# Kernel tuning notes

Hardware: AMD Instinct MI355X
Metric: run time of the kernel (lower is better)

## Reference

```python
import jax, jax.numpy as jnp
import numpy as np

B, N, C, CO = 256, 80, 1024, 1024
SLOPE = 0.2
BN_EPS = 1e-5

def leaky(x):
    return jax.nn.leaky_relu(x, SLOPE)

def setup_inputs() -> dict:
    key = jax.random.key(0)
    ks = jax.random.split(key, 8)
    stdv = 1.0 / np.sqrt(C)
    return {
        "x": jax.random.normal(ks[0], (B, N, C), jnp.float32),
        "out1": jax.random.normal(ks[1], (B, N), jnp.float32),
        "A": jax.random.uniform(ks[2], (N, N), jnp.float32, 0.05, 1.0),
        "static_weight": jax.random.uniform(ks[3], (C, C), jnp.float32, -stdv, stdv),
        "conv_g_w": jax.random.normal(ks[4], (C, C), jnp.float32) * 0.02,
        "conv_g_b": jnp.zeros((C,), jnp.float32),
        "bn_gamma": jnp.ones((C,), jnp.float32),
        "bn_beta": jnp.zeros((C,), jnp.float32),
        "conv_co_w": jax.random.normal(ks[5], (N, 2 * C), jnp.float32) * 0.02,
        "conv_co_b": jnp.zeros((N,), jnp.float32),
        "dynamic_weight": jax.random.uniform(ks[6], (C, CO), jnp.float32, -stdv, stdv),
    }

def _gen_adj(A):
    # D = diag(rowsum(A)^-0.5); adj = (A @ D).T @ D = D A^T D
    d = jnp.power(A.sum(1), -0.5)
    return d[:, None] * A.T * d[None, :]

def _gen_adjs(A):
    # batched version of _gen_adj; A: [B,N,N]
    d = jnp.power(A.sum(2), -0.5)  # [B,N]
    return d[:, :, None] * jnp.swapaxes(A, 1, 2) * d[:, None, :]

def reference(x, out1, A, static_weight, conv_g_w, conv_g_b, bn_gamma, bn_beta, conv_co_w, conv_co_b, dynamic_weight):
    n = x.shape[1]
    # static GCN + residual
    adj_s = _gen_adj(A)
    h = leaky(jnp.einsum('ij,bjc->bic', adj_s, x))
    x = x + h @ static_weight
    # construct dynamic graph
    xt = jnp.swapaxes(x, 1, 2)                      # [B,C,N]
    glb = xt.mean(2)                                # adaptive avg pool -> [B,C]
    glb = glb @ conv_g_w.T + conv_g_b               # 1x1 conv
    mu = glb.mean(0)
    var = glb.var(0)                                # biased, training-mode BN
    glb = (glb - mu) * jax.lax.rsqrt(var + BN_EPS) * bn_gamma + bn_beta
    glb = leaky(glb)
    cat = jnp.concatenate([jnp.broadcast_to(glb[:, :, None], xt.shape), xt], axis=1)  # [B,2C,N]
    dyn = jax.nn.sigmoid(jnp.einsum('nk,bkm->bnm', conv_co_w, cat) + conv_co_b[None, :, None])  # [B,N,N]
    # adjacency consistency loss
    out1s = jax.nn.sigmoid(out1)
    t = jnp.einsum('bn,bnm->bm', out1s, dyn) / n
    loss = jnp.sum(jnp.linalg.norm(out1s - t, axis=1))
    # dynamic GCN
    adjs = _gen_adjs(dyn)
    h = leaky(jnp.einsum('bnm,bmc->bnc', adjs, x))
    out = leaky(h @ dynamic_weight)
    return out, loss
```

## Files before the change

kernel.cpp:

```cpp
#include <hip/hip_runtime.h>
#include <hip/hip_bf16.h>
#include <math.h>

#define B_  256
#define N_  80
#define C_  1024
#define CO_ 1024

typedef __hip_bfloat16 bf16;
using bf16x8 = __attribute__((ext_vector_type(8))) short;
using f32x4  = __attribute__((ext_vector_type(4))) float;

__device__ __forceinline__ float leaky(float v){ return v >= 0.f ? v : 0.2f * v; }
__device__ __forceinline__ float sigmoidf_(float v){ return 1.f / (1.f + __expf(-v)); }

__device__ __forceinline__ void gll16(const void* g, void* l){
    __builtin_amdgcn_global_load_lds(
        (const __attribute__((address_space(1))) void*)g,
        (__attribute__((address_space(3))) void*)l, 16, 0, 0);
}

__global__ __launch_bounds__(256) void k_convT2(const float* __restrict__ W0, const float* __restrict__ W1,
                                                bf16* __restrict__ T0, bf16* __restrict__ T1){
    __shared__ float t[32][33];
    const float* W = blockIdx.z ? W1 : W0;
    bf16* WT = blockIdx.z ? T1 : T0;
    int k0 = blockIdx.y * 32, n0 = blockIdx.x * 32;
    int tx = threadIdx.x & 31, ty = threadIdx.x >> 5;
    for (int i = ty; i < 32; i += 8) t[i][tx] = W[(size_t)(k0 + i) * 1024 + n0 + tx];
    __syncthreads();
    for (int i = ty; i < 32; i += 8)
        WT[(size_t)(n0 + i) * 1024 + k0 + tx] = __float2bfloat16(t[tx][i]);
}

__global__ void k_cvt_ccw(const float* __restrict__ ccw, bf16* __restrict__ ccwb){
    int i = blockIdx.x * 256 + threadIdx.x;
    ccwb[i] = __float2bfloat16(ccw[i]);
}
__global__ void k_cvt4(const float* __restrict__ src, bf16* __restrict__ dst){
    int i = (blockIdx.x * 256 + threadIdx.x) * 4;
    float4 v = *(const float4*)(src + i);
    dst[i + 0] = __float2bfloat16(v.x);
    dst[i + 1] = __float2bfloat16(v.y);
    dst[i + 2] = __float2bfloat16(v.z);
    dst[i + 3] = __float2bfloat16(v.w);
}

__global__ void k_adj(const float* __restrict__ A, bf16* __restrict__ adjb){
    __shared__ float d[N_];
    int t = threadIdx.x;
    if (t < N_){
        float s = 0.f;
        for (int j = 0; j < N_; j++) s += A[t * N_ + j];
        d[t] = rsqrtf(s);
    }
    __syncthreads();
    for (int idx = t; idx < N_ * N_; idx += 256){
        int i = idx / N_, j = idx - i * N_;
        adjb[i * 88 + j] = __float2bfloat16(d[i] * A[j * N_ + i] * d[j]);
    }
}

__global__ __launch_bounds__(128) void k_prop_static(const float* __restrict__ xsrc,
                                                     const bf16* __restrict__ Ag,
                                                     bf16* __restrict__ H){
    __shared__ bf16 Btl[128 * 88];
    __shared__ bf16 Al [80 * 88];
    int b = blockIdx.x, c0 = blockIdx.y * 128, tid = threadIdx.x;
    int wave = tid >> 6, lane = tid & 63;
    int l15 = lane & 15, hi = lane >> 4;

    #pragma unroll
    for (int k = 0; k < 7; k++){
        int cb = k * 128 + wave * 64;
        if (cb + lane < 880)
            gll16(Ag + (size_t)(cb + lane) * 8, Al + (size_t)cb * 8);
    }
    {
        size_t rowbase = (size_t)b * 81920 + c0 + tid;
        #pragma unroll 8
        for (int m = 0; m < 80; m++)
            Btl[tid * 88 + m] = __float2bfloat16(xsrc[rowbase + (size_t)m * 1024]);
    }
    __syncthreads();

    f32x4 acc[5][4];
    #pragma unroll
    for (int i = 0; i < 5; i++)
        #pragma unroll
        for (int j = 0; j < 4; j++) acc[i][j] = (f32x4){0.f, 0.f, 0.f, 0.f};

    #pragma unroll
    for (int ks = 0; ks < 3; ks++){
        bf16x8 a[5], bv[4];
        if (ks < 2){
            int k0 = ks * 32;
            #pragma unroll
            for (int i = 0; i < 5; i++)
                a[i] = *(const bf16x8*)(Al + (i * 16 + l15) * 88 + k0 + hi * 8);
            #pragma unroll
            for (int j = 0; j < 4; j++)
                bv[j] = *(const bf16x8*)(Btl + (wave * 64 + j * 16 + l15) * 88 + k0 + hi * 8);
        } else {
            int koff = (hi < 2) ? 64 + hi * 8 : 0;
            #pragma unroll
            for (int i = 0; i < 5; i++){
                bf16x8 v = *(const bf16x8*)(Al + (i * 16 + l15) * 88 + koff);
                if (hi >= 2) v = 0;
                a[i] = v;
            }
            #pragma unroll
            for (int j = 0; j < 4; j++){
                bf16x8 v = *(const bf16x8*)(Btl + (wave * 64 + j * 16 + l15) * 88 + koff);
                if (hi >= 2) v = 0;
                bv[j] = v;
            }
        }
        #pragma unroll
        for (int i = 0; i < 5; i++)
            #pragma unroll
            for (int j = 0; j < 4; j++)
                acc[i][j] = __builtin_amdgcn_mfma_f32_16x16x32_bf16(a[i], bv[j], acc[i][j], 0, 0, 0);
    }

    #pragma unroll
    for (int i = 0; i < 5; i++){
        #pragma unroll
        for (int r = 0; r < 4; r++){
            int orow = i * 16 + hi * 4 + r;
            #pragma unroll
            for (int j = 0; j < 4; j++){
                int ocol = c0 + wave * 64 + j * 16 + l15;
                H[(size_t)b * 81920 + (size_t)orow * 1024 + ocol] =
                    __float2bfloat16(leaky(acc[i][j][r]));
            }
        }
    }
}

template<int EPI>
__global__ __launch_bounds__(256, 4) void k_gemm_mfma(const bf16* __restrict__ Abf,
                                                      const bf16* __restrict__ WT,
                                                      const float* __restrict__ Res,
                                                      void* __restrict__ Outv){
    __shared__ alignas(16) bf16 As[3][128 * 32];
    __shared__ alignas(16) bf16 Bs[2][128 * 32];
    const int K = 1024;
    const int NT = 32;
    int tid = threadIdx.x;
    int wave = tid >> 6, lane = tid & 63;
    int l15 = lane & 15, hi = lane >> 4;

    int bid = blockIdx.x;
    int xcd = bid & 7, idx = bid >> 3;
    int row0 = (xcd * 20 + (idx >> 3)) * 128;
    int col0 = (idx & 7) * 128;

    int sr = tid >> 2;
    int sq = (tid & 3) ^ ((tid >> 3) & 3);
    const bf16* gA = Abf + (size_t)(row0 + sr) * K + sq * 8;
    const bf16* gB = WT  + (size_t)(col0 + sr) * K + sq * 8;

    int wr = (wave >> 1) * 64, wc = (wave & 1) * 64;
    int soff = (hi ^ ((l15 >> 1) & 3)) * 8;

    f32x4 acc[4][4];
    #pragma unroll
    for (int i = 0; i < 4; i++)
        #pragma unroll
        for (int j = 0; j < 4; j++) acc[i][j] = (f32x4){0.f, 0.f, 0.f, 0.f};

    auto STAGE_A = [&](int t){
        bf16* da = &As[t % 3][wave * 512];
        gll16(gA + t * 32, da);
        gll16(gA + (size_t)64 * K + t * 32, da + 2048);
    };
    auto STAGE_B = [&](int t){
        bf16* db = &Bs[t & 1][wave * 512];
        gll16(gB + t * 32, db);
        gll16(gB + (size_t)64 * K + t * 32, db + 2048);
    };

    STAGE_A(0); STAGE_B(0); STAGE_A(1);
    for (int t = 0; t < NT; ++t){
        if (t < NT - 1) asm volatile("s_waitcnt vmcnt(2)" ::: "memory");
        else            asm volatile("s_waitcnt vmcnt(0)" ::: "memory");
        __builtin_amdgcn_s_barrier();
        if (t + 1 < NT) STAGE_B(t + 1);
        if (t + 2 < NT) STAGE_A(t + 2);
        const bf16* pa = &As[t % 3][0] + (wr + l15) * 32 + soff;
        const bf16* pb = &Bs[t & 1][0] + (wc + l15) * 32 + soff;
        bf16x8 a[4], b[4];
        #pragma unroll
        for (int i = 0; i < 4; i++) a[i] = *(const bf16x8*)(pa + i * 512);
        #pragma unroll
        for (int j = 0; j < 4; j++) b[j] = *(const bf16x8*)(pb + j * 512);
        __builtin_amdgcn_s_setprio(1);
        #pragma unroll
        for (int i = 0; i < 4; i++)
            #pragma unroll
            for (int j = 0; j < 4; j++)
                acc[i][j] = __builtin_amdgcn_mfma_f32_16x16x32_bf16(a[i], b[j], acc[i][j], 0, 0, 0);
        __builtin_amdgcn_s_setprio(0);
    }

    int orow = row0 + wr + hi * 4;
    int ocol = col0 + wc + l15;
    #pragma unroll
    for (int i = 0; i < 4; i++){
        #pragma unroll
        for (int r = 0; r < 4; r++){
            int rr = orow + i * 16 + r;
            #pragma unroll
            for (int j = 0; j < 4; j++){
                size_t o = (size_t)rr * 1024 + ocol + j * 16;
                float v = acc[i][j][r];
                if (EPI == 0) ((bf16*)Outv)[o] = __float2bfloat16(v + Res[o]);
                else          ((float*)Outv)[o] = leaky(v);
            }
        }
    }
}

__global__ __launch_bounds__(256) void k_gemm_glb(const bf16* __restrict__ Abf,
                                                  const bf16* __restrict__ Bw,
                                                  const float* __restrict__ bias,
                                                  float* __restrict__ Out){
    __shared__ alignas(16) bf16 As[3][128 * 32];
    __shared__ alignas(16) bf16 Bs[3][128 * 32];
    const int K = 1024;
    const int NT = 32;
    int tid = threadIdx.x;
    int wave = tid >> 6, lane = tid & 63;
    int l15 = lane & 15, hi = lane >> 4;

    int row0 = (blockIdx.x >> 3) * 128;
    int col0 = (blockIdx.x & 7) * 128;

    int sr = tid >> 2;
    int sq = (tid & 3) ^ ((tid >> 3) & 3);
    const bf16* gA = Abf + (size_t)(row0 + sr) * K + sq * 8;
    const bf16* gB = Bw  + (size_t)(col0 + sr) * K + sq * 8;

    int wr = (wave >> 1) * 64, wc = (wave & 1) * 64;
    int soff = (hi ^ ((l15 >> 1) & 3)) * 8;

    f32x4 acc[4][4];
    #pragma unroll
    for (int i = 0; i < 4; i++)
        #pragma unroll
        for (int j = 0; j < 4; j++) acc[i][j] = (f32x4){0.f, 0.f, 0.f, 0.f};

    auto STAGE = [&](int t){
        int buf = t % 3;
        int k0 = t * 32;
        bf16* da = &As[buf][wave * 512];
        bf16* db = &Bs[buf][wave * 512];
        gll16(gA + k0, da);
        gll16(gA + (size_t)64 * K + k0, da + 2048);
        gll16(gB + k0, db);
        gll16(gB + (size_t)64 * K + k0, db + 2048);
    };

    STAGE(0);
    STAGE(1);
    for (int t = 0; t < NT; ++t){
        if (t == NT - 1) asm volatile("s_waitcnt vmcnt(0)" ::: "memory");
        else             asm volatile("s_waitcnt vmcnt(4)" ::: "memory");
        __builtin_amdgcn_s_barrier();
        if (t + 2 < NT) STAGE(t + 2);
        int buf = t % 3;
        const bf16* pa = &As[buf][0] + (wr + l15) * 32 + soff;
        const bf16* pb = &Bs[buf][0] + (wc + l15) * 32 + soff;
        bf16x8 a[4], b[4];
        #pragma unroll
        for (int i = 0; i < 4; i++) a[i] = *(const bf16x8*)(pa + i * 512);
        #pragma unroll
        for (int j = 0; j < 4; j++) b[j] = *(const bf16x8*)(pb + j * 512);
        #pragma unroll
        for (int i = 0; i < 4; i++)
            #pragma unroll
            for (int j = 0; j < 4; j++)
                acc[i][j] = __builtin_amdgcn_mfma_f32_16x16x32_bf16(a[i], b[j], acc[i][j], 0, 0, 0);
    }

    int orow = row0 + wr + hi * 4;
    int ocol = col0 + wc + l15;
    #pragma unroll
    for (int i = 0; i < 4; i++){
        #pragma unroll
        for (int r = 0; r < 4; r++){
            int rr = orow + i * 16 + r;
            #pragma unroll
            for (int j = 0; j < 4; j++){
                int cl = ocol + j * 16;
                Out[(size_t)rr * 1024 + cl] = acc[i][j][r] + bias[cl];
            }
        }
    }
}

__global__ __launch_bounds__(128) void k_pool(const bf16* __restrict__ X2b, bf16* __restrict__ glb0b){
    int b = blockIdx.x, c8 = threadIdx.x * 8;
    const bf16* p = X2b + (size_t)b * 81920 + c8;
    float s[8] = {0.f,0.f,0.f,0.f,0.f,0.f,0.f,0.f};
    #pragma unroll 8
    for (int nn = 0; nn < N_; nn++){
        union { bf16x8 v; bf16 e[8]; } u;
        u.v = *(const bf16x8*)(p + (size_t)nn * 1024);
        #pragma unroll
        for (int k = 0; k < 8; k++) s[k] += __bfloat162float(u.e[k]);
    }
    #pragma unroll
    for (int k = 0; k < 8; k++)
        glb0b[b * C_ + c8 + k] = __float2bfloat16(s[k] * (1.f / N_));
}

__global__ __launch_bounds__(256) void k_bnstat(const float* __restrict__ g, float* __restrict__ mu,
                                                float* __restrict__ rstd){
    __shared__ float rs[8][32], rs2[8][32];
    int tid = threadIdx.x;
    int c = blockIdx.x * 32 + (tid & 31);
    int grp = tid >> 5;
    float s = 0.f, s2 = 0.f;
    for (int bb = 0; bb < 32; bb++){
        float v = g[(size_t)(grp * 32 + bb) * 1024 + c];
        s += v; s2 += v * v;
    }
    rs[grp][tid & 31] = s;
    rs2[grp][tid & 31] = s2;
    __syncthreads();
    if (tid < 32){
        float S = 0.f, S2 = 0.f;
        #pragma unroll
        for (int q = 0; q < 8; q++){ S += rs[q][tid]; S2 += rs2[q][tid]; }
        float m = S * (1.f / B_);
        float var = S2 * (1.f / B_) - m * m;
        int cc = blockIdx.x * 32 + tid;
        mu[cc] = m;
        rstd[cc] = rsqrtf(var + 1e-5f);
    }
}

__global__ void k_bnapply(const float* __restrict__ g, const float* __restrict__ mu,
                          const float* __restrict__ rstd, const float* __restrict__ gamma,
                          const float* __restrict__ beta, bf16* __restrict__ o){
    int i = blockIdx.x * 256 + threadIdx.x;
    int c = i & (C_ - 1);
    float v = (g[i] - mu[c]) * rstd[c] * gamma[c] + beta[c];
    o[i] = __float2bfloat16(leaky(v));
}

__global__ __launch_bounds__(512) void k_dyn_prop(const bf16* __restrict__ X2b,
                                                  const bf16* __restrict__ ccwb,
                                                  const bf16* __restrict__ glb2b,
                                                  const float* __restrict__ ccb,
                                                  const float* __restrict__ out1,
                                                  bf16* __restrict__ H,
                                                  float* __restrict__ lossp){
    __shared__ char uSb[80 * 81 * 4];
    __shared__ bf16 ADJ[80 * 90];
    __shared__ float di_s[80], o1s[80], dd[80];
    float* S = (float*)uSb;
    bf16* Btl = (bf16*)uSb;
    int b = blockIdx.x, tid = threadIdx.x;
    int wave = tid >> 6, lane = tid & 63;
    int l15 = lane & 15, hi = lane >> 4;

    if (wave < 5){
        const bf16* arow = ccwb + (size_t)(wave * 16 + l15) * 2048 + hi * 8;
        const bf16* gG = glb2b + (size_t)b * 1024 + hi * 8;
        const bf16* gX = X2b + (size_t)b * 81920 + hi * 8;
        f32x4 acc[5];
        #pragma unroll
        for (int j = 0; j < 5; j++) acc[j] = (f32x4){0.f, 0.f, 0.f, 0.f};
        #pragma unroll 8
        for (int k0 = 0; k0 < 1024; k0 += 32){
            bf16x8 a = *(const bf16x8*)(arow + k0);
            bf16x8 g = *(const bf16x8*)(gG + k0);
            #pragma unroll
            for (int j = 0; j < 5; j++)
                acc[j] = __builtin_amdgcn_mfma_f32_16x16x32_bf16(a, g, acc[j], 0, 0, 0);
        }
        #pragma unroll 4
        for (int k0 = 0; k0 < 1024; k0 += 32){
            bf16x8 a = *(const bf16x8*)(arow + 1024 + k0);
            #pragma unroll
            for (int j = 0; j < 5; j++){
                bf16x8 bv = *(const bf16x8*)(gX + (size_t)(j * 16 + l15) * 1024 + k0);
                acc[j] = __builtin_amdgcn_mfma_f32_16x16x32_bf16(a, bv, acc[j], 0, 0, 0);
            }
        }
        #pragma unroll
        for (int r = 0; r < 4; r++){
            int n = wave * 16 + hi * 4 + r;
            float cb = ccb[n];
            #pragma unroll
            for (int j = 0; j < 5; j++)
                S[n * 81 + j * 16 + l15] = sigmoidf_(acc[j][r] + cb);
        }
    }
    __syncthreads();
    if (tid < 80){
        float rsum = 0.f;
        #pragma unroll 8
        for (int m = 0; m < 80; m++) rsum += S[tid * 81 + m];
        di_s[tid] = rsqrtf(rsum);
        o1s[tid] = sigmoidf_(out1[b * 80 + tid]);
    }
    __syncthreads();
    if (tid < 80){
        float cs = 0.f;
        #pragma unroll 8
        for (int n = 0; n < 80; n++) cs += o1s[n] * S[n * 81 + tid];
        float diff = o1s[tid] - cs * (1.f / 80.f);
        dd[tid] = diff * diff;
    }
    __syncthreads();
    for (int idx = tid; idx < 6400; idx += 512){
        int n = idx / 80, m = idx - n * 80;
        ADJ[n * 90 + m] = __float2bfloat16(di_s[n] * S[m * 81 + n] * di_s[m]);
    }
    if (tid == 0){
        float s = 0.f;
        for (int m = 0; m < 80; m++) s += dd[m];
        lossp[b] = sqrtf(s);
    }
    for (int c0 = 0; c0 < 1024; c0 += 128){
        __syncthreads();
        {
            int cc = tid & 127, g = tid >> 7;
            const bf16* src = X2b + (size_t)b * 81920 + c0 + cc;
            #pragma unroll 5
            for (int m = g * 20; m < g * 20 + 20; m++)
                Btl[cc * 90 + m] = src[(size_t)m * 1024];
        }
        __syncthreads();
        f32x4 pacc[5];
        #pragma unroll
        for (int i = 0; i < 5; i++) pacc[i] = (f32x4){0.f, 0.f, 0.f, 0.f};
        #pragma unroll
        for (int ks = 0; ks < 3; ks++){
            int koff = (ks < 2) ? ks * 32 + hi * 8 : ((hi < 2) ? 64 + hi * 8 : 0);
            bool dead = (ks == 2) && (hi >= 2);
            bf16x8 bv = *(const bf16x8*)(Btl + (wave * 16 + l15) * 90 + koff);
            if (dead) bv = 0;
            #pragma unroll
            for (int i = 0; i < 5; i++){
                bf16x8 a = *(const bf16x8*)(ADJ + (i * 16 + l15) * 90 + koff);
                if (dead) a = 0;
                pacc[i] = __builtin_amdgcn_mfma_f32_16x16x32_bf16(a, bv, pacc[i], 0, 0, 0);
            }
        }
        #pragma unroll
        for (int i = 0; i < 5; i++){
            #pragma unroll
            for (int r = 0; r < 4; r++){
                int n = i * 16 + hi * 4 + r;
                int col = c0 + wave * 16 + l15;
                H[(size_t)b * 81920 + (size_t)n * 1024 + col] =
                    __float2bfloat16(leaky(pacc[i][r]));
            }
        }
    }
}

__global__ void k_lsum(const float* __restrict__ lossp, float* __restrict__ out_loss){
    float v = lossp[threadIdx.x];
    for (int off = 32; off; off >>= 1) v += __shfl_down(v, off);
    __shared__ float wsum[4];
    int lane = threadIdx.x & 63, w = threadIdx.x >> 6;
    if (lane == 0) wsum[w] = v;
    __syncthreads();
    if (threadIdx.x == 0) out_loss[0] = wsum[0] + wsum[1] + wsum[2] + wsum[3];
}

extern "C" void kernel_launch(void* const* d_in, const int* in_sizes, int n_in,
                              void* d_out, int out_size, void* d_ws, size_t ws_size,
                              hipStream_t stream) {
    const float* x     = (const float*)d_in[0];
    const float* out1  = (const float*)d_in[1];
    const float* A     = (const float*)d_in[2];
    const float* sw    = (const float*)d_in[3];
    const float* cgw   = (const float*)d_in[4];
    const float* cgb   = (const float*)d_in[5];
    const float* gamma = (const float*)d_in[6];
    const float* beta  = (const float*)d_in[7];
    const float* ccw   = (const float*)d_in[8];
    const float* ccb   = (const float*)d_in[9];
    const float* dw    = (const float*)d_in[10];
    float* out = (float*)d_out;

    const size_t XN = (size_t)B_ * N_ * C_;
    char* p = (char*)d_ws;
    bf16*  Hbf  = (bf16*)p;   p += XN * 2;
    bf16*  X2b  = (bf16*)p;   p += XN * 2;
    bf16*  SWT  = (bf16*)p;   p += (size_t)C_ * C_ * 2;
    bf16*  DWT  = (bf16*)p;   p += (size_t)C_ * CO_ * 2;
    bf16*  CCWB = (bf16*)p;   p += (size_t)N_ * 2048 * 2;
    bf16*  CGWB = (bf16*)p;   p += (size_t)C_ * C_ * 2;
    bf16*  ADJS = (bf16*)p;   p += (size_t)80 * 88 * 2;
    bf16*  GLB0 = (bf16*)p;   p += (size_t)B_ * C_ * 2;
    float* GLB1 = (float*)p;  p += (size_t)B_ * C_ * 4;
    bf16*  GLB2 = (bf16*)p;   p += (size_t)B_ * C_ * 2;
    float* MU   = (float*)p;  p += C_ * 4;
    float* RSTD = (float*)p;  p += C_ * 4;
    float* LOSSP= (float*)p;  p += B_ * 4;

    k_convT2<<<dim3(32, 32, 2), 256, 0, stream>>>(sw, dw, SWT, DWT);
    k_cvt_ccw<<<(N_ * 2048) / 256, 256, 0, stream>>>(ccw, CCWB);
    k_cvt4<<<(C_ * C_) / 1024, 256, 0, stream>>>(cgw, CGWB);
    k_adj<<<1, 256, 0, stream>>>(A, ADJS);
    k_prop_static<<<dim3(B_, 8), 128, 0, stream>>>(x, ADJS, Hbf);
    k_gemm_mfma<0><<<1280, 256, 0, stream>>>(Hbf, SWT, x, X2b);
    k_pool<<<B_, 128, 0, stream>>>(X2b, GLB0);
    k_gemm_glb<<<16, 256, 0, stream>>>(GLB0, CGWB, cgb, GLB1);
    k_bnstat<<<32, 256, 0, stream>>>(GLB1, MU, RSTD);
    k_bnapply<<<(B_ * C_) / 256, 256, 0, stream>>>(GLB1, MU, RSTD, gamma, beta, GLB2);
    k_dyn_prop<<<B_, 512, 0, stream>>>(X2b, CCWB, GLB2, ccb, out1, Hbf, LOSSP);
    k_lsum<<<1, 256, 0, stream>>>(LOSSP, out + (size_t)B_ * N_ * CO_);
    k_gemm_mfma<1><<<1280, 256, 0, stream>>>(Hbf, DWT, nullptr, out);
}
```

Before: 271.9 us.

## Use 256x256 GEMM tiles with 8 waves and interleaved quarter-tile staging

```diff
diff --git a/kernel.cpp b/kernel.cpp
--- a/kernel.cpp
+++ b/kernel.cpp
@@ -139,75 +139,120 @@
 }
 
 template<int EPI>
-__global__ __launch_bounds__(256, 4) void k_gemm_mfma(const bf16* __restrict__ Abf,
-                                                      const bf16* __restrict__ WT,
-                                                      const float* __restrict__ Res,
-                                                      void* __restrict__ Outv){
-    __shared__ alignas(16) bf16 As[3][128 * 32];
-    __shared__ alignas(16) bf16 Bs[2][128 * 32];
+__global__ __launch_bounds__(512, 1) void k_gemm_256(const bf16* __restrict__ Abf,
+                                                     const bf16* __restrict__ WT,
+                                                     const float* __restrict__ Res,
+                                                     void* __restrict__ Outv){
+    __shared__ alignas(16) bf16 As[3][256 * 32];
+    __shared__ alignas(16) bf16 Bs[3][256 * 32];
     const int K = 1024;
     const int NT = 32;
     int tid = threadIdx.x;
     int wave = tid >> 6, lane = tid & 63;
     int l15 = lane & 15, hi = lane >> 4;
+    int wm = wave >> 2, wn = wave & 3;
 
     int bid = blockIdx.x;
     int xcd = bid & 7, idx = bid >> 3;
-    int row0 = (xcd * 20 + (idx >> 3)) * 128;
-    int col0 = (idx & 7) * 128;
+    int row0 = (xcd * 10 + (idx >> 2)) * 256;
+    int col0 = (idx & 3) * 256;
 
     int sr = tid >> 2;
     int sq = (tid & 3) ^ ((tid >> 3) & 3);
-    const bf16* gA = Abf + (size_t)(row0 + sr) * K + sq * 8;
-    const bf16* gB = WT  + (size_t)(col0 + sr) * K + sq * 8;
-
-    int wr = (wave >> 1) * 64, wc = (wave & 1) * 64;
+    int wbase = wave * 512;
+
     int soff = (hi ^ ((l15 >> 1) & 3)) * 8;
 
-    f32x4 acc[4][4];
-    #pragma unroll
-    for (int i = 0; i < 4; i++)
+    f32x4 acc[8][4];
+    #pragma unroll
+    for (int i = 0; i < 8; i++)
         #pragma unroll
         for (int j = 0; j < 4; j++) acc[i][j] = (f32x4){0.f, 0.f, 0.f, 0.f};
 
-    auto STAGE_A = [&](int t){
-        bf16* da = &As[t % 3][wave * 512];
-        gll16(gA + t * 32, da);
-        gll16(gA + (size_t)64 * K + t * 32, da + 2048);
+    auto STAGE_HT = [&](int kt, int buf, int ht){
+        const bf16* srcb;
+        bf16* dst;
+        if      (ht == 0){ srcb = Abf + (size_t)(row0 + sr) * K;       dst = &As[buf][0];    }
+        else if (ht == 1){ srcb = Abf + (size_t)(row0 + 128 + sr) * K; dst = &As[buf][4096]; }
+        else if (ht == 2){ srcb = WT  + (size_t)(col0 + sr) * K;       dst = &Bs[buf][0];    }
+        else             { srcb = WT  + (size_t)(col0 + 128 + sr) * K; dst = &Bs[buf][4096]; }
+        gll16(srcb + kt * 32 + sq * 8, dst + wbase);
     };
-    auto STAGE_B = [&](int t){
-        bf16* db = &Bs[t & 1][wave * 512];
-        gll16(gB + t * 32, db);
-        gll16(gB + (size_t)64 * K + t * 32, db + 2048);
-    };
-
-    STAGE_A(0); STAGE_B(0); STAGE_A(1);
-    for (int t = 0; t < NT; ++t){
-        if (t < NT - 1) asm volatile("s_waitcnt vmcnt(2)" ::: "memory");
-        else            asm volatile("s_waitcnt vmcnt(0)" ::: "memory");
-        __builtin_amdgcn_s_barrier();
-        if (t + 1 < NT) STAGE_B(t + 1);
-        if (t + 2 < NT) STAGE_A(t + 2);
-        const bf16* pa = &As[t % 3][0] + (wr + l15) * 32 + soff;
-        const bf16* pb = &Bs[t & 1][0] + (wc + l15) * 32 + soff;
-        bf16x8 a[4], b[4];
-        #pragma unroll
-        for (int i = 0; i < 4; i++) a[i] = *(const bf16x8*)(pa + i * 512);
-        #pragma unroll
-        for (int j = 0; j < 4; j++) b[j] = *(const bf16x8*)(pb + j * 512);
+
+    #pragma unroll
+    for (int ht = 0; ht < 4; ht++) STAGE_HT(0, 0, ht);
+    #pragma unroll
+    for (int ht = 0; ht < 4; ht++) STAGE_HT(1, 1, ht);
+    asm volatile("s_waitcnt vmcnt(4)" ::: "memory");
+    __builtin_amdgcn_s_barrier();
+
+    int buf = 0, sbuf = 2;
+    for (int kt = 0; kt < NT; ++kt){
+        const bf16* SA = &As[buf][0];
+        const bf16* SB = &Bs[buf][0];
+        bool st = (kt + 2 < NT);
+        bf16x8 a[4], b0[2], b1[2];
+
+        if (st) STAGE_HT(kt + 2, sbuf, 0);
+        #pragma unroll
+        for (int i = 0; i < 4; i++)
+            a[i] = *(const bf16x8*)(SA + (wm * 128 + i * 16 + l15) * 32 + soff);
+        #pragma unroll
+        for (int j = 0; j < 2; j++)
+            b0[j] = *(const bf16x8*)(SB + (wn * 64 + j * 16 + l15) * 32 + soff);
         __builtin_amdgcn_s_setprio(1);
         #pragma unroll
         for (int i = 0; i < 4; i++)
             #pragma unroll
-            for (int j = 0; j < 4; j++)
-                acc[i][j] = __builtin_amdgcn_mfma_f32_16x16x32_bf16(a[i], b[j], acc[i][j], 0, 0, 0);
+            for (int j = 0; j < 2; j++)
+                acc[i][j] = __builtin_amdgcn_mfma_f32_16x16x32_bf16(a[i], b0[j], acc[i][j], 0, 0, 0);
         __builtin_amdgcn_s_setprio(0);
-    }
-
-    int orow = row0 + wr + hi * 4;
-    int ocol = col0 + wc + l15;
-    #pragma unroll
-    for (int i = 0; i < 4; i++){
+
+        if (st) STAGE_HT(kt + 2, sbuf, 1);
+        #pragma unroll
+        for (int j = 0; j < 2; j++)
+            b1[j] = *(const bf16x8*)(SB + (wn * 64 + 32 + j * 16 + l15) * 32 + soff);
+        __builtin_amdgcn_s_setprio(1);
+        #pragma unroll
+        for (int i = 0; i < 4; i++)
+            #pragma unroll
+            for (int j = 0; j < 2; j++)
+                acc[i][2 + j] = __builtin_amdgcn_mfma_f32_16x16x32_bf16(a[i], b1[j], acc[i][2 + j], 0, 0, 0);
+        __builtin_amdgcn_s_setprio(0);
+
+        if (st) STAGE_HT(kt + 2, sbuf, 2);
+        #pragma unroll
+        for (int i = 0; i < 4; i++)
+            a[i] = *(const bf16x8*)(SA + (wm * 128 + 64 + i * 16 + l15) * 32 + soff);
+        __builtin_amdgcn_s_setprio(1);
+        #pragma unroll
+        for (int i = 0; i < 4; i++)
+            #pragma unroll
+            for (int j = 0; j < 2; j++)
+                acc[4 + i][2 + j] = __builtin_amdgcn_mfma_f32_16x16x32_bf16(a[i], b1[j], acc[4 + i][2 + j], 0, 0, 0);
+        __builtin_amdgcn_s_setprio(0);
+
+        if (st) STAGE_HT(kt + 2, sbuf, 3);
+        __builtin_amdgcn_s_setprio(1);
+        #pragma unroll
+        for (int i = 0; i < 4; i++)
+            #pragma unroll
+            for (int j = 0; j < 2; j++)
+                acc[4 + i][j] = __builtin_amdgcn_mfma_f32_16x16x32_bf16(a[i], b0[j], acc[4 + i][j], 0, 0, 0);
+        __builtin_amdgcn_s_setprio(0);
+
+        if (st) asm volatile("s_waitcnt vmcnt(4)" ::: "memory");
+        else    asm volatile("s_waitcnt vmcnt(0)" ::: "memory");
+        if (kt + 1 < NT) __builtin_amdgcn_s_barrier();
+
+        buf  = (buf  == 2) ? 0 : buf  + 1;
+        sbuf = (sbuf == 2) ? 0 : sbuf + 1;
+    }
+
+    int orow = row0 + wm * 128 + hi * 4;
+    int ocol = col0 + wn * 64 + l15;
+    #pragma unroll
+    for (int i = 0; i < 8; i++){
         #pragma unroll
         for (int r = 0; r < 4; r++){
             int rr = orow + i * 16 + r;
@@ -512,12 +557,12 @@
     k_cvt4<<<(C_ * C_) / 1024, 256, 0, stream>>>(cgw, CGWB);
     k_adj<<<1, 256, 0, stream>>>(A, ADJS);
     k_prop_static<<<dim3(B_, 8), 128, 0, stream>>>(x, ADJS, Hbf);
-    k_gemm_mfma<0><<<1280, 256, 0, stream>>>(Hbf, SWT, x, X2b);
+    k_gemm_256<0><<<320, 512, 0, stream>>>(Hbf, SWT, x, X2b);
     k_pool<<<B_, 128, 0, stream>>>(X2b, GLB0);
     k_gemm_glb<<<16, 256, 0, stream>>>(GLB0, CGWB, cgb, GLB1);
     k_bnstat<<<32, 256, 0, stream>>>(GLB1, MU, RSTD);
     k_bnapply<<<(B_ * C_) / 256, 256, 0, stream>>>(GLB1, MU, RSTD, gamma, beta, GLB2);
     k_dyn_prop<<<B_, 512, 0, stream>>>(X2b, CCWB, GLB2, ccb, out1, Hbf, LOSSP);
     k_lsum<<<1, 256, 0, stream>>>(LOSSP, out + (size_t)B_ * N_ * CO_);
-    k_gemm_mfma<1><<<1280, 256, 0, stream>>>(Hbf, DWT, nullptr, out);
-}
+    k_gemm_256<1><<<320, 512, 0, stream>>>(Hbf, DWT, nullptr, out);
+}
```

Result: slower. 339.1 us (+24.8%).
